# Performance work log

Measured on AMD Instinct MI355X. Metric: run time of the kernel, lower is better.

Reference implementation:

```python
import jax, jax.numpy as jnp
import numpy as np

NSITES = 100000
NYEARS = 20
NVIS = 2
HDIM = 64


def setup_inputs() -> dict:
    key = jax.random.key(0)
    ks = jax.random.split(key, 10)
    def w(k, shape, fan_in):
        return (jax.random.normal(k, shape, jnp.float32) / np.sqrt(fan_in)).astype(jnp.float32)
    return {
        "sxy0": jax.random.normal(ks[0], (1, NSITES, 1), jnp.float32),
        "sxy": jax.random.normal(ks[1], (NSITES, NYEARS - 1, 1), jnp.float32),
        "oxy": jax.random.normal(ks[2], (NSITES, NYEARS, NVIS), jnp.float32),
        # to_h0: Linear(1 -> 64)
        "W_h0": w(ks[3], (HDIM, 1), 1), "b_h0": jnp.zeros((HDIM,), jnp.float32),
        # to_h1: Linear(64 -> 64)
        "W_h1": w(ks[4], (HDIM, HDIM), HDIM), "b_h1": jnp.zeros((HDIM,), jnp.float32),
        # to_hrnn: RNN(input=1, hidden=64, relu)
        "W_ih": w(ks[5], (HDIM, 1), 1), "b_ih": jnp.zeros((HDIM,), jnp.float32),
        "W_hh": w(ks[6], (HDIM, HDIM), HDIM), "b_hh": jnp.zeros((HDIM,), jnp.float32),
        # to_psi0 / to_psi: Linear(64 -> 1)
        "W_psi0": w(ks[7], (1, HDIM), HDIM), "b_psi0": jnp.zeros((1,), jnp.float32),
        "W_psi": w(ks[8], (1, HDIM), HDIM), "b_psi": jnp.zeros((1,), jnp.float32),
        # to_p: Linear(65 -> 1)
        "W_p": w(ks[9], (1, HDIM + 1), HDIM + 1), "b_p": jnp.zeros((1,), jnp.float32),
    }


def reference(sxy0, sxy, oxy, W_h0, b_h0, W_h1, b_h1, W_ih, b_ih, W_hh, b_hh,
              W_psi0, b_psi0, W_psi, b_psi, W_p, b_p):
    # site embeddings -> initial hidden state
    hs = jax.nn.elu(sxy0 @ W_h0.T + b_h0)            # [1, N, H]
    h0 = jax.nn.elu(hs @ W_h1.T + b_h1)              # [1, N, H]

    # single-layer relu RNN, batch_first: sxy [N, T, 1], h0 [1, N, H]
    xs = jnp.swapaxes(sxy, 0, 1)                     # [T, N, 1]
    def step(h, x):
        h_new = jax.nn.relu(x @ W_ih.T + b_ih + h @ W_hh.T + b_hh)
        return h_new, h_new
    _, h_seq = jax.lax.scan(step, h0[0], xs)         # [T, N, H]
    h_out = jnp.swapaxes(h_seq, 0, 1)                # [N, T, H]

    psi0_out = jax.nn.sigmoid(h0 @ W_psi0.T + b_psi0)   # [1, N, 1]
    psi_out = jax.nn.sigmoid(h_out @ W_psi.T + b_psi)   # [N, T, 1]

    # detection prob p[i, t, j] = sigmoid(to_p(cat(H[i, t], oxy[i, t, j])))
    # where H[:, 0] = h0 and H[:, t] = h_out[:, t-1] for t >= 1
    H = jnp.concatenate([h0[0][:, None, :], h_out], axis=1)  # [N, Y, H]
    logits = H @ W_p[:, :HDIM].T + oxy * W_p[0, HDIM] + b_p  # [N, Y, NVIS]
    p = jax.nn.sigmoid(logits)
    return psi0_out, psi_out, p
```

## Files before the change

kernel.cpp:

```cpp
#include <hip/hip_runtime.h>
#include <math.h>

#define NSITES 100000
#define NYEARS 20
#define HDIM 64

typedef __bf16 bf16x8 __attribute__((ext_vector_type(8)));
typedef float f32x4 __attribute__((ext_vector_type(4)));

__device__ __forceinline__ float sigmoidf_(float x) { return 1.0f / (1.0f + __expf(-x)); }
__device__ __forceinline__ float eluf_(float x) { return x > 0.0f ? x : expm1f(x); }

__device__ __forceinline__ bf16x8 cvt8_(const float* p) {
    float4 a = ((const float4*)p)[0];
    float4 b = ((const float4*)p)[1];
    bf16x8 r;
    r[0] = (__bf16)a.x; r[1] = (__bf16)a.y; r[2] = (__bf16)a.z; r[3] = (__bf16)a.w;
    r[4] = (__bf16)b.x; r[5] = (__bf16)b.y; r[6] = (__bf16)b.z; r[7] = (__bf16)b.w;
    return r;
}

__device__ __forceinline__ bf16x8 pack_bf_(f32x4 lo, f32x4 hi) {
    bf16x8 r;
    r[0] = (__bf16)lo[0]; r[1] = (__bf16)lo[1]; r[2] = (__bf16)lo[2]; r[3] = (__bf16)lo[3];
    r[4] = (__bf16)hi[0]; r[5] = (__bf16)hi[1]; r[6] = (__bf16)hi[2]; r[7] = (__bf16)hi[3];
    return r;
}

__global__ __launch_bounds__(64, 2)
void rnet_kernel(const float* __restrict__ sxy0,
                 const float* __restrict__ sxy,
                 const float* __restrict__ oxy,
                 const float* __restrict__ W_h0, const float* __restrict__ b_h0,
                 const float* __restrict__ W_h1, const float* __restrict__ b_h1,
                 const float* __restrict__ W_ih, const float* __restrict__ b_ih,
                 const float* __restrict__ W_hh, const float* __restrict__ b_hh,
                 const float* __restrict__ W_psi0, const float* __restrict__ b_psi0,
                 const float* __restrict__ W_psi, const float* __restrict__ b_psi,
                 const float* __restrict__ W_p, const float* __restrict__ b_p,
                 float* __restrict__ out)
{
    const int lane = threadIdx.x;
    const int s = lane & 15;
    const int q = lane >> 4;
    const int sq = s >> 2, sr = s & 3;
    const int base = blockIdx.x * 16;
    const int site = base + s;

    __shared__ __align__(16) float pL_sh[16 * 20];
    __shared__ __align__(16) float psiL_sh[16 * 19];

    float* __restrict__ out_psi0 = out;
    float* __restrict__ out_psi  = out + NSITES;
    float* __restrict__ out_p    = out + 20 * NSITES;

    bf16x8 a_hh[4][2];
#pragma unroll
    for (int mt = 0; mt < 4; ++mt) {
        const int ar = 32 * (mt >> 1) + 8 * sq + 4 * (mt & 1) + sr;
#pragma unroll
        for (int kt = 0; kt < 2; ++kt)
            a_hh[mt][kt] = cvt8_(W_hh + ar * 64 + kt * 32 + q * 8);
    }
    bf16x8 a_head[2];
    {
        const float* hrow = (s == 1) ? W_p : ((s == 2) ? W_psi0 : W_psi);
#pragma unroll
        for (int kt = 0; kt < 2; ++kt) a_head[kt] = cvt8_(hrow + kt * 32 + q * 8);
    }

    f32x4 biasD[4], wihD[4];
#pragma unroll
    for (int mt = 0; mt < 4; ++mt) {
        const int dr = 32 * (mt >> 1) + 8 * q + 4 * (mt & 1);
        float4 bi = *(const float4*)(b_ih + dr);
        float4 bh = *(const float4*)(b_hh + dr);
        float4 wi = *(const float4*)(W_ih + dr);
        biasD[mt][0] = bi.x + bh.x; biasD[mt][1] = bi.y + bh.y;
        biasD[mt][2] = bi.z + bh.z; biasD[mt][3] = bi.w + bh.w;
        wihD[mt][0] = wi.x; wihD[mt][1] = wi.y; wihD[mt][2] = wi.z; wihD[mt][3] = wi.w;
    }
    f32x4 headC;
    headC[0] = (q == 0) ? b_psi[0]  : 0.0f;
    headC[1] = (q == 0) ? b_p[0]    : 0.0f;
    headC[2] = (q == 0) ? b_psi0[0] : 0.0f;
    headC[3] = 0.0f;
    const float wpo = W_p[HDIM];

    float xs[NYEARS - 1];
    {
        const float* sxy_l = sxy + (size_t)site * (NYEARS - 1);
#pragma unroll
        for (int i = 0; i < NYEARS - 1; ++i) xs[i] = sxy_l[i];
    }

    bf16x8 bf[2];
    {
        const float s0v = sxy0[site];
        bf16x8 bf0[2];
#pragma unroll
        for (int kt = 0; kt < 2; ++kt) {
            const float* wp = W_h0 + kt * 32 + q * 8;
            const float* bp = b_h0 + kt * 32 + q * 8;
            float4 w0 = ((const float4*)wp)[0], w1 = ((const float4*)wp)[1];
            float4 c0 = ((const float4*)bp)[0], c1 = ((const float4*)bp)[1];
            float v[8];
            v[0] = eluf_(fmaf(s0v, w0.x, c0.x)); v[1] = eluf_(fmaf(s0v, w0.y, c0.y));
            v[2] = eluf_(fmaf(s0v, w0.z, c0.z)); v[3] = eluf_(fmaf(s0v, w0.w, c0.w));
            v[4] = eluf_(fmaf(s0v, w1.x, c1.x)); v[5] = eluf_(fmaf(s0v, w1.y, c1.y));
            v[6] = eluf_(fmaf(s0v, w1.z, c1.z)); v[7] = eluf_(fmaf(s0v, w1.w, c1.w));
#pragma unroll
            for (int j = 0; j < 8; ++j) bf0[kt][j] = (__bf16)v[j];
        }

        f32x4 acc[4];
#pragma unroll
        for (int mt = 0; mt < 4; ++mt) {
            const int dr = 32 * (mt >> 1) + 8 * q + 4 * (mt & 1);
            float4 b1 = *(const float4*)(b_h1 + dr);
            acc[mt][0] = b1.x; acc[mt][1] = b1.y; acc[mt][2] = b1.z; acc[mt][3] = b1.w;
        }
#pragma unroll
        for (int kt = 0; kt < 2; ++kt)
#pragma unroll
            for (int mt = 0; mt < 4; ++mt) {
                const int ar = 32 * (mt >> 1) + 8 * sq + 4 * (mt & 1) + sr;
                bf16x8 a = cvt8_(W_h1 + ar * 64 + kt * 32 + q * 8);
                acc[mt] = __builtin_amdgcn_mfma_f32_16x16x32_bf16(a, bf0[kt], acc[mt], 0, 0, 0);
            }
        f32x4 e[4];
#pragma unroll
        for (int mt = 0; mt < 4; ++mt)
#pragma unroll
            for (int r = 0; r < 4; ++r) e[mt][r] = eluf_(acc[mt][r]);
        bf[0] = pack_bf_(e[0], e[1]);
        bf[1] = pack_bf_(e[2], e[3]);
    }

#pragma unroll
    for (int t = 1; t < NYEARS; ++t) {
        f32x4 acc[4], accH = headC;
#pragma unroll
        for (int mt = 0; mt < 4; ++mt) acc[mt] = biasD[mt];
#pragma unroll
        for (int kt = 0; kt < 2; ++kt) {
#pragma unroll
            for (int mt = 0; mt < 4; ++mt)
                acc[mt] = __builtin_amdgcn_mfma_f32_16x16x32_bf16(a_hh[mt][kt], bf[kt], acc[mt], 0, 0, 0);
            accH = __builtin_amdgcn_mfma_f32_16x16x32_bf16(a_head[kt], bf[kt], accH, 0, 0, 0);
        }

        const float x = xs[t - 1];
        f32x4 hn[4];
#pragma unroll
        for (int mt = 0; mt < 4; ++mt)
#pragma unroll
            for (int r = 0; r < 4; ++r)
                hn[mt][r] = fmaxf(fmaf(x, wihD[mt][r], acc[mt][r]), 0.0f);
        bf[0] = pack_bf_(hn[0], hn[1]);
        bf[1] = pack_bf_(hn[2], hn[3]);

        if (q == 0) {
            pL_sh[s * 20 + (t - 1)] = accH[1];
            if (t == 1) {
                out_psi0[site] = sigmoidf_(accH[2]);
            } else {
                psiL_sh[s * 19 + (t - 2)] = accH[0];
            }
        }
    }

    {
        f32x4 accH = headC;
#pragma unroll
        for (int kt = 0; kt < 2; ++kt)
            accH = __builtin_amdgcn_mfma_f32_16x16x32_bf16(a_head[kt], bf[kt], accH, 0, 0, 0);
        if (q == 0) {
            pL_sh[s * 20 + 19] = accH[1];
            psiL_sh[s * 19 + 18] = accH[0];
        }
    }

    __syncthreads();

#pragma unroll
    for (int r = 0; r < 5; ++r) {
        int i = r * 64 + lane;
        if (i < 16 * 19)
            out_psi[(size_t)base * 19 + i] = sigmoidf_(psiL_sh[i]);
    }
    const float* oxy_b = oxy + (size_t)base * 40;
    float* outp_b = out_p + (size_t)base * 40;
#pragma unroll
    for (int r = 0; r < 10; ++r) {
        int i = r * 64 + lane;
        float lg = pL_sh[i >> 1];
        outp_b[i] = sigmoidf_(fmaf(wpo, oxy_b[i], lg));
    }
}

extern "C" void kernel_launch(void* const* d_in, const int* in_sizes, int n_in,
                              void* d_out, int out_size, void* d_ws, size_t ws_size,
                              hipStream_t stream) {
    const float* sxy0   = (const float*)d_in[0];
    const float* sxy    = (const float*)d_in[1];
    const float* oxy    = (const float*)d_in[2];
    const float* W_h0   = (const float*)d_in[3];
    const float* b_h0   = (const float*)d_in[4];
    const float* W_h1   = (const float*)d_in[5];
    const float* b_h1   = (const float*)d_in[6];
    const float* W_ih   = (const float*)d_in[7];
    const float* b_ih   = (const float*)d_in[8];
    const float* W_hh   = (const float*)d_in[9];
    const float* b_hh   = (const float*)d_in[10];
    const float* W_psi0 = (const float*)d_in[11];
    const float* b_psi0 = (const float*)d_in[12];
    const float* W_psi  = (const float*)d_in[13];
    const float* b_psi  = (const float*)d_in[14];
    const float* W_p    = (const float*)d_in[15];
    const float* b_p    = (const float*)d_in[16];

    float* out = (float*)d_out;

    dim3 block(64);
    dim3 grid(NSITES / 16);
    rnet_kernel<<<grid, block, 0, stream>>>(
        sxy0, sxy, oxy, W_h0, b_h0, W_h1, b_h1, W_ih, b_ih, W_hh, b_hh,
        W_psi0, b_psi0, W_psi, b_psi, W_p, b_p, out);
}
```

Baseline: 152.7 us.

## Process two 16-site groups per wavefront to interleave MFMA recurrence chains

Each 64-thread block now handles 32 sites as two independent 16-site groups, issuing their RNN MFMAs interleaved. This hides MFMA latency along the serial time recurrence and amortises the per-block weight fragment loads over twice the sites. The output p stage is also vectorised to float4 loads and stores. The cost is higher register use per lane and half as many blocks, which may lower occupancy.

```diff
diff --git a/kernel.cpp b/kernel.cpp
--- a/kernel.cpp
+++ b/kernel.cpp
@@ -44,11 +44,12 @@
     const int s = lane & 15;
     const int q = lane >> 4;
     const int sq = s >> 2, sr = s & 3;
-    const int base = blockIdx.x * 16;
-    const int site = base + s;
-
-    __shared__ __align__(16) float pL_sh[16 * 20];
-    __shared__ __align__(16) float psiL_sh[16 * 19];
+    const int base = blockIdx.x * 32;
+    const int site0 = base + s;
+    const int site1 = base + 16 + s;
+
+    __shared__ __align__(16) float pL_sh[32 * 20];
+    __shared__ __align__(16) float psiL_sh[32 * 19];
 
     float* __restrict__ out_psi0 = out;
     float* __restrict__ out_psi  = out + NSITES;
@@ -87,38 +88,48 @@
     headC[3] = 0.0f;
     const float wpo = W_p[HDIM];
 
-    float xs[NYEARS - 1];
+    float xs[2][NYEARS - 1];
+#pragma unroll
+    for (int i = 0; i < NYEARS - 1; ++i) {
+        xs[0][i] = sxy[(size_t)site0 * (NYEARS - 1) + i];
+        xs[1][i] = sxy[(size_t)site1 * (NYEARS - 1) + i];
+    }
+
+    bf16x8 bf[2][2];
     {
-        const float* sxy_l = sxy + (size_t)site * (NYEARS - 1);
-#pragma unroll
-        for (int i = 0; i < NYEARS - 1; ++i) xs[i] = sxy_l[i];
-    }
-
-    bf16x8 bf[2];
-    {
-        const float s0v = sxy0[site];
-        bf16x8 bf0[2];
+        float s0v[2];
+        s0v[0] = sxy0[site0];
+        s0v[1] = sxy0[site1];
+        bf16x8 bf0[2][2];
 #pragma unroll
         for (int kt = 0; kt < 2; ++kt) {
             const float* wp = W_h0 + kt * 32 + q * 8;
             const float* bp = b_h0 + kt * 32 + q * 8;
             float4 w0 = ((const float4*)wp)[0], w1 = ((const float4*)wp)[1];
             float4 c0 = ((const float4*)bp)[0], c1 = ((const float4*)bp)[1];
-            float v[8];
-            v[0] = eluf_(fmaf(s0v, w0.x, c0.x)); v[1] = eluf_(fmaf(s0v, w0.y, c0.y));
-            v[2] = eluf_(fmaf(s0v, w0.z, c0.z)); v[3] = eluf_(fmaf(s0v, w0.w, c0.w));
-            v[4] = eluf_(fmaf(s0v, w1.x, c1.x)); v[5] = eluf_(fmaf(s0v, w1.y, c1.y));
-            v[6] = eluf_(fmaf(s0v, w1.z, c1.z)); v[7] = eluf_(fmaf(s0v, w1.w, c1.w));
-#pragma unroll
-            for (int j = 0; j < 8; ++j) bf0[kt][j] = (__bf16)v[j];
-        }
-
-        f32x4 acc[4];
+#pragma unroll
+            for (int g = 0; g < 2; ++g) {
+                const float sv = s0v[g];
+                float v[8];
+                v[0] = eluf_(fmaf(sv, w0.x, c0.x)); v[1] = eluf_(fmaf(sv, w0.y, c0.y));
+                v[2] = eluf_(fmaf(sv, w0.z, c0.z)); v[3] = eluf_(fmaf(sv, w0.w, c0.w));
+                v[4] = eluf_(fmaf(sv, w1.x, c1.x)); v[5] = eluf_(fmaf(sv, w1.y, c1.y));
+                v[6] = eluf_(fmaf(sv, w1.z, c1.z)); v[7] = eluf_(fmaf(sv, w1.w, c1.w));
+#pragma unroll
+                for (int j = 0; j < 8; ++j) bf0[g][kt][j] = (__bf16)v[j];
+            }
+        }
+
+        f32x4 acc[2][4];
 #pragma unroll
         for (int mt = 0; mt < 4; ++mt) {
             const int dr = 32 * (mt >> 1) + 8 * q + 4 * (mt & 1);
             float4 b1 = *(const float4*)(b_h1 + dr);
-            acc[mt][0] = b1.x; acc[mt][1] = b1.y; acc[mt][2] = b1.z; acc[mt][3] = b1.w;
+#pragma unroll
+            for (int g = 0; g < 2; ++g) {
+                acc[g][mt][0] = b1.x; acc[g][mt][1] = b1.y;
+                acc[g][mt][2] = b1.z; acc[g][mt][3] = b1.w;
+            }
         }
 #pragma unroll
         for (int kt = 0; kt < 2; ++kt)
@@ -126,76 +137,102 @@
             for (int mt = 0; mt < 4; ++mt) {
                 const int ar = 32 * (mt >> 1) + 8 * sq + 4 * (mt & 1) + sr;
                 bf16x8 a = cvt8_(W_h1 + ar * 64 + kt * 32 + q * 8);
-                acc[mt] = __builtin_amdgcn_mfma_f32_16x16x32_bf16(a, bf0[kt], acc[mt], 0, 0, 0);
-            }
-        f32x4 e[4];
-#pragma unroll
-        for (int mt = 0; mt < 4; ++mt)
-#pragma unroll
-            for (int r = 0; r < 4; ++r) e[mt][r] = eluf_(acc[mt][r]);
-        bf[0] = pack_bf_(e[0], e[1]);
-        bf[1] = pack_bf_(e[2], e[3]);
+#pragma unroll
+                for (int g = 0; g < 2; ++g)
+                    acc[g][mt] = __builtin_amdgcn_mfma_f32_16x16x32_bf16(a, bf0[g][kt], acc[g][mt], 0, 0, 0);
+            }
+#pragma unroll
+        for (int g = 0; g < 2; ++g) {
+            f32x4 e[4];
+#pragma unroll
+            for (int mt = 0; mt < 4; ++mt)
+#pragma unroll
+                for (int r = 0; r < 4; ++r) e[mt][r] = eluf_(acc[g][mt][r]);
+            bf[g][0] = pack_bf_(e[0], e[1]);
+            bf[g][1] = pack_bf_(e[2], e[3]);
+        }
     }
 
 #pragma unroll
     for (int t = 1; t < NYEARS; ++t) {
-        f32x4 acc[4], accH = headC;
-#pragma unroll
-        for (int mt = 0; mt < 4; ++mt) acc[mt] = biasD[mt];
+        f32x4 acc[2][4], accH[2];
+#pragma unroll
+        for (int g = 0; g < 2; ++g) {
+            accH[g] = headC;
+#pragma unroll
+            for (int mt = 0; mt < 4; ++mt) acc[g][mt] = biasD[mt];
+        }
 #pragma unroll
         for (int kt = 0; kt < 2; ++kt) {
 #pragma unroll
             for (int mt = 0; mt < 4; ++mt)
-                acc[mt] = __builtin_amdgcn_mfma_f32_16x16x32_bf16(a_hh[mt][kt], bf[kt], acc[mt], 0, 0, 0);
-            accH = __builtin_amdgcn_mfma_f32_16x16x32_bf16(a_head[kt], bf[kt], accH, 0, 0, 0);
-        }
-
-        const float x = xs[t - 1];
-        f32x4 hn[4];
-#pragma unroll
-        for (int mt = 0; mt < 4; ++mt)
-#pragma unroll
-            for (int r = 0; r < 4; ++r)
-                hn[mt][r] = fmaxf(fmaf(x, wihD[mt][r], acc[mt][r]), 0.0f);
-        bf[0] = pack_bf_(hn[0], hn[1]);
-        bf[1] = pack_bf_(hn[2], hn[3]);
-
+#pragma unroll
+                for (int g = 0; g < 2; ++g)
+                    acc[g][mt] = __builtin_amdgcn_mfma_f32_16x16x32_bf16(a_hh[mt][kt], bf[g][kt], acc[g][mt], 0, 0, 0);
+#pragma unroll
+            for (int g = 0; g < 2; ++g)
+                accH[g] = __builtin_amdgcn_mfma_f32_16x16x32_bf16(a_head[kt], bf[g][kt], accH[g], 0, 0, 0);
+        }
+
+#pragma unroll
+        for (int g = 0; g < 2; ++g) {
+            const float x = xs[g][t - 1];
+            f32x4 hn[4];
+#pragma unroll
+            for (int mt = 0; mt < 4; ++mt)
+#pragma unroll
+                for (int r = 0; r < 4; ++r)
+                    hn[mt][r] = fmaxf(fmaf(x, wihD[mt][r], acc[g][mt][r]), 0.0f);
+            bf[g][0] = pack_bf_(hn[0], hn[1]);
+            bf[g][1] = pack_bf_(hn[2], hn[3]);
+
+            if (q == 0) {
+                const int ls = g * 16 + s;
+                pL_sh[ls * 20 + (t - 1)] = accH[g][1];
+                if (t == 1) {
+                    out_psi0[base + g * 16 + s] = sigmoidf_(accH[g][2]);
+                } else {
+                    psiL_sh[ls * 19 + (t - 2)] = accH[g][0];
+                }
+            }
+        }
+    }
+
+#pragma unroll
+    for (int g = 0; g < 2; ++g) {
+        f32x4 accH = headC;
+#pragma unroll
+        for (int kt = 0; kt < 2; ++kt)
+            accH = __builtin_amdgcn_mfma_f32_16x16x32_bf16(a_head[kt], bf[g][kt], accH, 0, 0, 0);
         if (q == 0) {
-            pL_sh[s * 20 + (t - 1)] = accH[1];
-            if (t == 1) {
-                out_psi0[site] = sigmoidf_(accH[2]);
-            } else {
-                psiL_sh[s * 19 + (t - 2)] = accH[0];
-            }
-        }
-    }
-
-    {
-        f32x4 accH = headC;
-#pragma unroll
-        for (int kt = 0; kt < 2; ++kt)
-            accH = __builtin_amdgcn_mfma_f32_16x16x32_bf16(a_head[kt], bf[kt], accH, 0, 0, 0);
-        if (q == 0) {
-            pL_sh[s * 20 + 19] = accH[1];
-            psiL_sh[s * 19 + 18] = accH[0];
+            const int ls = g * 16 + s;
+            pL_sh[ls * 20 + 19] = accH[1];
+            psiL_sh[ls * 19 + 18] = accH[0];
         }
     }
 
     __syncthreads();
 
-#pragma unroll
-    for (int r = 0; r < 5; ++r) {
-        int i = r * 64 + lane;
-        if (i < 16 * 19)
-            out_psi[(size_t)base * 19 + i] = sigmoidf_(psiL_sh[i]);
-    }
-    const float* oxy_b = oxy + (size_t)base * 40;
-    float* outp_b = out_p + (size_t)base * 40;
 #pragma unroll
     for (int r = 0; r < 10; ++r) {
         int i = r * 64 + lane;
-        float lg = pL_sh[i >> 1];
-        outp_b[i] = sigmoidf_(fmaf(wpo, oxy_b[i], lg));
+        if (i < 32 * 19)
+            out_psi[(size_t)base * 19 + i] = sigmoidf_(psiL_sh[i]);
+    }
+    const float4* oxy_b = (const float4*)(oxy + (size_t)base * 40);
+    float4* outp_b = (float4*)(out_p + (size_t)base * 40);
+#pragma unroll
+    for (int r = 0; r < 5; ++r) {
+        int i4 = r * 64 + lane;
+        float4 ox = oxy_b[i4];
+        float lg0 = pL_sh[i4 * 2];
+        float lg1 = pL_sh[i4 * 2 + 1];
+        float4 pv;
+        pv.x = sigmoidf_(fmaf(wpo, ox.x, lg0));
+        pv.y = sigmoidf_(fmaf(wpo, ox.y, lg0));
+        pv.z = sigmoidf_(fmaf(wpo, ox.z, lg1));
+        pv.w = sigmoidf_(fmaf(wpo, ox.w, lg1));
+        outp_b[i4] = pv;
     }
 }
 
@@ -223,7 +260,7 @@
     float* out = (float*)d_out;
 
     dim3 block(64);
-    dim3 grid(NSITES / 16);
+    dim3 grid(NSITES / 32);
     rnet_kernel<<<grid, block, 0, stream>>>(
         sxy0, sxy, oxy, W_h0, b_h0, W_h1, b_h1, W_ih, b_ih, W_hh, b_hh,
         W_psi0, b_psi0, W_psi, b_psi, W_p, b_p, out);
```

Measured after the change: 149.4 us. 2.2% less time.

## Cut register pressure for higher occupancy and vectorize the epilogue stores

Applied to the files above, without the earlier changes.

Raises the launch bound from 2 to 4 waves per SIMD and lowers register pressure to fit it. The sxy inputs now go through shared memory with a coalesced load, the weight fragments are loaded after the h0 computation, and the time loop is no longer unrolled. The psi/psi0 writes are deferred to a shared-memory epilogue, and the oxy/p epilogue uses float4 loads and stores. The goal is more waves in flight to hide MFMA and memory latency, at the cost of loop overhead and extra LDS traffic inside the recurrence.

```diff
diff --git a/kernel.cpp b/kernel.cpp
--- a/kernel.cpp
+++ b/kernel.cpp
@@ -27,7 +27,7 @@
     return r;
 }
 
-__global__ __launch_bounds__(64, 2)
+__global__ __launch_bounds__(64, 4)
 void rnet_kernel(const float* __restrict__ sxy0,
                  const float* __restrict__ sxy,
                  const float* __restrict__ oxy,
@@ -47,51 +47,22 @@
     const int base = blockIdx.x * 16;
     const int site = base + s;
 
+    __shared__ __align__(16) float xs_sh[16 * 19];
     __shared__ __align__(16) float pL_sh[16 * 20];
-    __shared__ __align__(16) float psiL_sh[16 * 19];
+    __shared__ __align__(16) float psiL_sh[16 * 20];
+    __shared__ __align__(16) float psi0L_sh[16];
 
     float* __restrict__ out_psi0 = out;
     float* __restrict__ out_psi  = out + NSITES;
     float* __restrict__ out_p    = out + 20 * NSITES;
 
-    bf16x8 a_hh[4][2];
-#pragma unroll
-    for (int mt = 0; mt < 4; ++mt) {
-        const int ar = 32 * (mt >> 1) + 8 * sq + 4 * (mt & 1) + sr;
-#pragma unroll
-        for (int kt = 0; kt < 2; ++kt)
-            a_hh[mt][kt] = cvt8_(W_hh + ar * 64 + kt * 32 + q * 8);
-    }
-    bf16x8 a_head[2];
-    {
-        const float* hrow = (s == 1) ? W_p : ((s == 2) ? W_psi0 : W_psi);
-#pragma unroll
-        for (int kt = 0; kt < 2; ++kt) a_head[kt] = cvt8_(hrow + kt * 32 + q * 8);
-    }
-
-    f32x4 biasD[4], wihD[4];
-#pragma unroll
-    for (int mt = 0; mt < 4; ++mt) {
-        const int dr = 32 * (mt >> 1) + 8 * q + 4 * (mt & 1);
-        float4 bi = *(const float4*)(b_ih + dr);
-        float4 bh = *(const float4*)(b_hh + dr);
-        float4 wi = *(const float4*)(W_ih + dr);
-        biasD[mt][0] = bi.x + bh.x; biasD[mt][1] = bi.y + bh.y;
-        biasD[mt][2] = bi.z + bh.z; biasD[mt][3] = bi.w + bh.w;
-        wihD[mt][0] = wi.x; wihD[mt][1] = wi.y; wihD[mt][2] = wi.z; wihD[mt][3] = wi.w;
-    }
-    f32x4 headC;
-    headC[0] = (q == 0) ? b_psi[0]  : 0.0f;
-    headC[1] = (q == 0) ? b_p[0]    : 0.0f;
-    headC[2] = (q == 0) ? b_psi0[0] : 0.0f;
-    headC[3] = 0.0f;
-    const float wpo = W_p[HDIM];
-
-    float xs[NYEARS - 1];
-    {
-        const float* sxy_l = sxy + (size_t)site * (NYEARS - 1);
-#pragma unroll
-        for (int i = 0; i < NYEARS - 1; ++i) xs[i] = sxy_l[i];
+    {
+        const float* src = sxy + (size_t)base * (NYEARS - 1);
+#pragma unroll
+        for (int r = 0; r < 5; ++r) {
+            int i = r * 64 + lane;
+            if (i < 16 * (NYEARS - 1)) xs_sh[i] = src[i];
+        }
     }
 
     bf16x8 bf[2];
@@ -137,20 +108,51 @@
         bf[1] = pack_bf_(e[2], e[3]);
     }
 
-#pragma unroll
+    bf16x8 a_hh[4][2];
+#pragma unroll
+    for (int mt = 0; mt < 4; ++mt) {
+        const int ar = 32 * (mt >> 1) + 8 * sq + 4 * (mt & 1) + sr;
+#pragma unroll
+        for (int kt = 0; kt < 2; ++kt)
+            a_hh[mt][kt] = cvt8_(W_hh + ar * 64 + kt * 32 + q * 8);
+    }
+    bf16x8 a_head[2];
+    {
+        const float* hrow = (s == 1) ? W_p : ((s == 2) ? W_psi0 : W_psi);
+#pragma unroll
+        for (int kt = 0; kt < 2; ++kt) a_head[kt] = cvt8_(hrow + kt * 32 + q * 8);
+    }
+    f32x4 biasD[4], wihD[4];
+#pragma unroll
+    for (int mt = 0; mt < 4; ++mt) {
+        const int dr = 32 * (mt >> 1) + 8 * q + 4 * (mt & 1);
+        float4 bi = *(const float4*)(b_ih + dr);
+        float4 bh = *(const float4*)(b_hh + dr);
+        float4 wi = *(const float4*)(W_ih + dr);
+        biasD[mt][0] = bi.x + bh.x; biasD[mt][1] = bi.y + bh.y;
+        biasD[mt][2] = bi.z + bh.z; biasD[mt][3] = bi.w + bh.w;
+        wihD[mt][0] = wi.x; wihD[mt][1] = wi.y; wihD[mt][2] = wi.z; wihD[mt][3] = wi.w;
+    }
+    f32x4 headC;
+    headC[0] = (q == 0) ? b_psi[0]  : 0.0f;
+    headC[1] = (q == 0) ? b_p[0]    : 0.0f;
+    headC[2] = (q == 0) ? b_psi0[0] : 0.0f;
+    headC[3] = 0.0f;
+
+#pragma unroll 1
     for (int t = 1; t < NYEARS; ++t) {
-        f32x4 acc[4], accH = headC;
-#pragma unroll
-        for (int mt = 0; mt < 4; ++mt) acc[mt] = biasD[mt];
-#pragma unroll
-        for (int kt = 0; kt < 2; ++kt) {
-#pragma unroll
-            for (int mt = 0; mt < 4; ++mt)
-                acc[mt] = __builtin_amdgcn_mfma_f32_16x16x32_bf16(a_hh[mt][kt], bf[kt], acc[mt], 0, 0, 0);
-            accH = __builtin_amdgcn_mfma_f32_16x16x32_bf16(a_head[kt], bf[kt], accH, 0, 0, 0);
-        }
-
-        const float x = xs[t - 1];
+        const float x = xs_sh[s * 19 + (t - 1)];
+
+        f32x4 acc[4], accH;
+#pragma unroll
+        for (int mt = 0; mt < 4; ++mt)
+            acc[mt] = __builtin_amdgcn_mfma_f32_16x16x32_bf16(a_hh[mt][0], bf[0], biasD[mt], 0, 0, 0);
+        accH = __builtin_amdgcn_mfma_f32_16x16x32_bf16(a_head[0], bf[0], headC, 0, 0, 0);
+#pragma unroll
+        for (int mt = 0; mt < 4; ++mt)
+            acc[mt] = __builtin_amdgcn_mfma_f32_16x16x32_bf16(a_hh[mt][1], bf[1], acc[mt], 0, 0, 0);
+        accH = __builtin_amdgcn_mfma_f32_16x16x32_bf16(a_head[1], bf[1], accH, 0, 0, 0);
+
         f32x4 hn[4];
 #pragma unroll
         for (int mt = 0; mt < 4; ++mt)
@@ -161,41 +163,49 @@
         bf[1] = pack_bf_(hn[2], hn[3]);
 
         if (q == 0) {
-            pL_sh[s * 20 + (t - 1)] = accH[1];
-            if (t == 1) {
-                out_psi0[site] = sigmoidf_(accH[2]);
-            } else {
-                psiL_sh[s * 19 + (t - 2)] = accH[0];
-            }
-        }
-    }
-
-    {
-        f32x4 accH = headC;
-#pragma unroll
-        for (int kt = 0; kt < 2; ++kt)
-            accH = __builtin_amdgcn_mfma_f32_16x16x32_bf16(a_head[kt], bf[kt], accH, 0, 0, 0);
+            pL_sh[s * 20 + (t - 1)]   = accH[1];
+            psiL_sh[s * 20 + (t - 1)] = accH[0];
+            if (t == 1) psi0L_sh[s] = accH[2];
+        }
+    }
+
+    {
+        f32x4 accH = __builtin_amdgcn_mfma_f32_16x16x32_bf16(a_head[0], bf[0], headC, 0, 0, 0);
+        accH = __builtin_amdgcn_mfma_f32_16x16x32_bf16(a_head[1], bf[1], accH, 0, 0, 0);
         if (q == 0) {
-            pL_sh[s * 20 + 19] = accH[1];
-            psiL_sh[s * 19 + 18] = accH[0];
+            pL_sh[s * 20 + 19]   = accH[1];
+            psiL_sh[s * 20 + 19] = accH[0];
         }
     }
 
     __syncthreads();
 
+    const float wpo = W_p[HDIM];
+    if (lane < 16) out_psi0[base + lane] = sigmoidf_(psi0L_sh[lane]);
 #pragma unroll
     for (int r = 0; r < 5; ++r) {
         int i = r * 64 + lane;
-        if (i < 16 * 19)
-            out_psi[(size_t)base * 19 + i] = sigmoidf_(psiL_sh[i]);
-    }
-    const float* oxy_b = oxy + (size_t)base * 40;
-    float* outp_b = out_p + (size_t)base * 40;
-#pragma unroll
-    for (int r = 0; r < 10; ++r) {
-        int i = r * 64 + lane;
-        float lg = pL_sh[i >> 1];
-        outp_b[i] = sigmoidf_(fmaf(wpo, oxy_b[i], lg));
+        if (i < 16 * 19) {
+            int sl = i / 19, c = i - sl * 19;
+            out_psi[(size_t)base * 19 + i] = sigmoidf_(psiL_sh[sl * 20 + c + 1]);
+        }
+    }
+    const float4* oxy_b = (const float4*)(oxy + (size_t)base * 40);
+    float4* outp_b = (float4*)(out_p + (size_t)base * 40);
+#pragma unroll
+    for (int r = 0; r < 3; ++r) {
+        int i4 = r * 64 + lane;
+        if (i4 < 160) {
+            float4 ox = oxy_b[i4];
+            float lg0 = pL_sh[i4 * 2];
+            float lg1 = pL_sh[i4 * 2 + 1];
+            float4 pv;
+            pv.x = sigmoidf_(fmaf(wpo, ox.x, lg0));
+            pv.y = sigmoidf_(fmaf(wpo, ox.y, lg0));
+            pv.z = sigmoidf_(fmaf(wpo, ox.z, lg1));
+            pv.w = sigmoidf_(fmaf(wpo, ox.w, lg1));
+            outp_b[i4] = pv;
+        }
     }
 }
 
```

Measured after the change: 166.2 us. 1.09x slower.
